# Optimization experiments

Hardware: AMD Instinct MI355X
Metric: run time of the kernel (lower is better)

Reference implementation:

```python
import jax, jax.numpy as jnp
import numpy as np

B, N, F_IN, F_OUT = 64, 1024, 200, 200
NEG_SLOPE = 0.2  # PyG GATConv default


def setup_inputs() -> dict:
    key = jax.random.key(0)
    k1, k2, k3, k4, k5 = jax.random.split(key, 5)
    return {
        "x": jax.random.normal(k1, (B, 1, N, F_IN), dtype=jnp.float32),
        "W": jax.random.normal(k2, (F_IN, F_OUT), dtype=jnp.float32) * 0.05,
        "att_src": jax.random.normal(k3, (F_OUT,), dtype=jnp.float32) * 0.05,
        "att_dst": jax.random.normal(k4, (F_OUT,), dtype=jnp.float32) * 0.05,
        "bias": jax.random.normal(k5, (F_OUT,), dtype=jnp.float32) * 0.05,
    }


def reference(x, W, att_src, att_dst, bias):
    # x: [B, 1, N, F_IN]; module flattens to (B*N) nodes but the edge_index
    # only spans node ids 0..N-1 (complete graph minus self loops). PyG's
    # GATConv re-adds self loops for ALL B*N nodes, so:
    #   nodes 0..N-1 : dense softmax attention over all N nodes (incl. self)
    #   nodes >= N   : only the self loop -> out = h_i + bias
    b, _, n, f = x.shape
    xf = x.reshape(b * n, f)
    h = xf @ W                                # [B*N, F_OUT] linear transform

    h0 = h[:n]                                # first graph's nodes
    a_s = h0 @ att_src                        # [N] per-source score
    a_d = h0 @ att_dst                        # [N] per-target score
    # score[i, j] = leaky_relu(a_dst[i] + a_src[j]), softmax over sources j
    scores = jax.nn.leaky_relu(a_d[:, None] + a_s[None, :], negative_slope=NEG_SLOPE)
    alpha = jax.nn.softmax(scores, axis=1)    # [N, N]
    out0 = alpha @ h0 + bias                  # [N, F_OUT]

    out_rest = h[n:] + bias                   # self-loop only -> alpha == 1
    out = jnp.concatenate([out0, out_rest], axis=0)
    return out.reshape(b, n, -1)[:, None]     # [B, 1, N, F_OUT]
```

## Files before the change

kernel.cpp:

```cpp
#include <hip/hip_runtime.h>

#define BATCH 64
#define NNODE 1024
#define FDIM  200
#define MROWS (BATCH * NNODE)
#define NEG_SLOPE 0.2f

#define NKT 7
#define NNT 13

typedef short s16x8 __attribute__((ext_vector_type(8)));
typedef float f32x4 __attribute__((ext_vector_type(4)));


__device__ __forceinline__ unsigned int f2bf(float f) {
    unsigned int u = __float_as_uint(f);
    return (u + 0x7fffu + ((u >> 16) & 1u)) >> 16;
}
__device__ __forceinline__ unsigned int pack2(float a, float b) {
    return f2bf(a) | (f2bf(b) << 16);
}

__global__ __launch_bounds__(64) void k_prep(const float* __restrict__ W,
                                             const float* __restrict__ att_src,
                                             const float* __restrict__ att_dst,
                                             unsigned short* __restrict__ fragW,
                                             float* __restrict__ wsv,
                                             float* __restrict__ wdv)
{
    const int b    = blockIdx.x;
    const int lane = threadIdx.x;

    if (b < 91) {
        const int kt   = b / NNT;
        const int nt   = b - kt * NNT;
        const int n    = nt * 16 + (lane & 15);
        const int kb   = kt * 32 + (lane >> 4) * 8;
        s16x8 v;
        #pragma unroll
        for (int j = 0; j < 8; ++j) {
            int k = kb + j;
            float f = (k < FDIM && n < FDIM) ? W[k * FDIM + n] : 0.f;
            v[j] = (short)f2bf(f);
        }
        ((s16x8*)(fragW + (size_t)b * 512))[lane] = v;
    } else {
        const int kk = b - 91;
        const float* Wr = W + kk * FDIM;
        float ps = 0.f, pd = 0.f;
        #pragma unroll
        for (int i = 0; i < 4; ++i) {
            int n = lane + i * 64;
            if (n < FDIM) {
                float wv = Wr[n];
                ps = fmaf(wv, att_src[n], ps);
                pd = fmaf(wv, att_dst[n], pd);
            }
        }
        #pragma unroll
        for (int off = 32; off; off >>= 1) {
            ps += __shfl_down(ps, off);
            pd += __shfl_down(pd, off);
        }
        if (lane == 0) { wsv[kk] = ps; wdv[kk] = pd; }
    }
}

__global__ __launch_bounds__(256) void k_av(const float* __restrict__ x,
                                            const float* __restrict__ wsv,
                                            const float* __restrict__ wdv,
                                            float* __restrict__ a_s,
                                            float* __restrict__ a_d)
{
    const int tid  = threadIdx.x;
    const int lane = tid & 63;
    const int row  = blockIdx.x * 4 + (tid >> 6);
    const float* xr = x + (size_t)row * FDIM;
    float ss = 0.f, sd = 0.f;
    for (int k = lane; k < FDIM; k += 64) {
        float xv = xr[k];
        ss = fmaf(xv, wsv[k], ss);
        sd = fmaf(xv, wdv[k], sd);
    }
    #pragma unroll
    for (int off = 32; off; off >>= 1) {
        ss += __shfl_down(ss, off);
        sd += __shfl_down(sd, off);
    }
    if (lane == 0) { a_s[row] = ss; a_d[row] = sd; }
}

__global__ __launch_bounds__(64) void k_gemm(const float* __restrict__ x,
                                             const unsigned short* __restrict__ fragW,
                                             const float* __restrict__ bias,
                                             float* __restrict__ out,
                                             unsigned short* __restrict__ h0frag)
{
    __shared__ float scr[16][17];
    const int lane = threadIdx.x;
    const int ln   = lane & 15;
    const int quad = lane >> 4;
    const int R0   = blockIdx.x * 16;

    f32x4 acc[NNT];
    #pragma unroll
    for (int nt = 0; nt < NNT; ++nt) acc[nt] = (f32x4){0.f, 0.f, 0.f, 0.f};

    const float* xrow = x + (size_t)(R0 + ln) * FDIM;

    float4 ar[NKT][2];
    #pragma unroll
    for (int kt = 0; kt < 4; ++kt) {
        const float4* ap = (const float4*)(xrow + kt * 32 + quad * 8);
        ar[kt][0] = ap[0]; ar[kt][1] = ap[1];
    }

    s16x8 bc[NNT], bn[NNT];
    #pragma unroll
    for (int nt = 0; nt < NNT; ++nt)
        bc[nt] = *(const s16x8*)(fragW + ((size_t)nt * 64 + lane) * 8);

    #pragma unroll
    for (int kt = 0; kt < NKT; ++kt) {
        if (kt < NKT - 1) {
            #pragma unroll
            for (int nt = 0; nt < NNT; ++nt)
                bn[nt] = *(const s16x8*)(fragW +
                    ((size_t)((kt + 1) * NNT + nt) * 64 + lane) * 8);
        }
        if (kt + 4 < NKT) {
            int ka = kt + 4;
            if (ka < 6) {
                const float4* ap = (const float4*)(xrow + ka * 32 + quad * 8);
                ar[ka][0] = ap[0]; ar[ka][1] = ap[1];
            } else {
                if (quad == 0) {
                    const float4* ap = (const float4*)(xrow + ka * 32);
                    ar[ka][0] = ap[0]; ar[ka][1] = ap[1];
                } else {
                    ar[ka][0] = make_float4(0.f, 0.f, 0.f, 0.f);
                    ar[ka][1] = make_float4(0.f, 0.f, 0.f, 0.f);
                }
            }
        }
        float4 f0 = ar[kt][0], f1 = ar[kt][1];
        unsigned int au[4] = {pack2(f0.x, f0.y), pack2(f0.z, f0.w),
                              pack2(f1.x, f1.y), pack2(f1.z, f1.w)};
        s16x8 a = *(s16x8*)au;
        #pragma unroll
        for (int nt = 0; nt < NNT; ++nt)
            acc[nt] = __builtin_amdgcn_mfma_f32_16x16x32_bf16(a, bc[nt], acc[nt], 0, 0, 0);
        if (kt < NKT - 1) {
            #pragma unroll
            for (int nt = 0; nt < NNT; ++nt) bc[nt] = bn[nt];
        }
    }

    if (R0 >= NNODE) {
        #pragma unroll
        for (int nt = 0; nt < NNT; ++nt) {
            int col = nt * 16 + ln;
            if (nt < 12 || ln < 8) {
                float bv = bias[col];
                #pragma unroll
                for (int r = 0; r < 4; ++r)
                    out[(size_t)(R0 + quad * 4 + r) * FDIM + col] = acc[nt][r] + bv;
            }
        }
    } else {
        const int kt2 = R0 >> 5;
        const int lo  = (R0 >> 4) & 1;
        for (int nt = 0; nt < NNT; ++nt) {
            #pragma unroll
            for (int r = 0; r < 4; ++r) scr[quad * 4 + r][ln] = acc[nt][r];
            __syncthreads();
            if (lane < 32) {
                int oct = lane >> 4, nl = lane & 15;
                uint4 dv;
                dv.x = pack2(scr[oct * 8 + 0][nl], scr[oct * 8 + 1][nl]);
                dv.y = pack2(scr[oct * 8 + 2][nl], scr[oct * 8 + 3][nl]);
                dv.z = pack2(scr[oct * 8 + 4][nl], scr[oct * 8 + 5][nl]);
                dv.w = pack2(scr[oct * 8 + 6][nl], scr[oct * 8 + 7][nl]);
                *(uint4*)(h0frag + ((size_t)(kt2 * NNT + nt) * 64 + lo * 32 + lane) * 8) = dv;
            }
            __syncthreads();
        }
    }
}

__global__ __launch_bounds__(256) void k_stats(const float* __restrict__ a_s,
                                               const float* __restrict__ a_d,
                                               float* __restrict__ m_out,
                                               float* __restrict__ l_out)
{
    __shared__ float as_s[1024];
    const int tid = threadIdx.x;
    #pragma unroll
    for (int i = 0; i < 4; ++i) as_s[tid + i * 256] = a_s[tid + i * 256];
    __syncthreads();

    const int lane = tid & 63;
    const int row  = blockIdx.x * 4 + (tid >> 6);

    float mx = -1e30f;
    #pragma unroll
    for (int i = 0; i < 16; ++i) mx = fmaxf(mx, as_s[lane + i * 64]);
    #pragma unroll
    for (int off = 32; off; off >>= 1) mx = fmaxf(mx, __shfl_down(mx, off));
    mx = __shfl(mx, 0);

    const float ad = a_d[row];
    float mi = ad + mx; mi = (mi > 0.f) ? mi : NEG_SLOPE * mi;

    float sum = 0.f;
    #pragma unroll
    for (int i = 0; i < 16; ++i) {
        float s = ad + as_s[lane + i * 64];
        s = (s > 0.f) ? s : NEG_SLOPE * s;
        sum += __expf(s - mi);
    }
    #pragma unroll
    for (int off = 32; off; off >>= 1) sum += __shfl_down(sum, off);
    if (lane == 0) { m_out[row] = mi; l_out[row] = sum; }
}

__global__ __launch_bounds__(256) void k_attn(const unsigned short* __restrict__ h0frag,
                                              const float* __restrict__ a_s,
                                              const float* __restrict__ a_d,
                                              const float* __restrict__ m_v,
                                              const float* __restrict__ l_v,
                                              const float* __restrict__ bias,
                                              float* __restrict__ out)
{
    const int tid  = threadIdx.x;
    const int lane = tid & 63;
    const int w    = __builtin_amdgcn_readfirstlane(tid >> 6);
    const int ln   = lane & 15;
    const int quad = lane >> 4;
    const int it   = blockIdx.x / NNT;
    const int nt   = blockIdx.x - it * NNT;
    const int i0   = it * 64 + w * 16;

    const float ad = a_d[i0 + ln];
    const float mi = m_v[i0 + ln];

    f32x4 accA = (f32x4){0.f, 0.f, 0.f, 0.f};
    f32x4 accB = (f32x4){0.f, 0.f, 0.f, 0.f};

    #pragma unroll
    for (int kt2 = 0; kt2 < 32; ++kt2) {
        const float4* ap = (const float4*)(a_s + kt2 * 32 + quad * 8);
        float4 f0 = ap[0], f1 = ap[1];
        float e[8] = {f0.x, f0.y, f0.z, f0.w, f1.x, f1.y, f1.z, f1.w};
        #pragma unroll
        for (int j = 0; j < 8; ++j) {
            float s = ad + e[j];
            s = (s > 0.f) ? s : NEG_SLOPE * s;
            e[j] = __expf(s - mi);
        }
        unsigned int au[4] = {pack2(e[0], e[1]), pack2(e[2], e[3]),
                              pack2(e[4], e[5]), pack2(e[6], e[7])};
        s16x8 afrag = *(s16x8*)au;
        s16x8 b = *(const s16x8*)(h0frag + ((size_t)(kt2 * NNT + nt) * 64 + lane) * 8);
        if (kt2 & 1) accB = __builtin_amdgcn_mfma_f32_16x16x32_bf16(afrag, b, accB, 0, 0, 0);
        else         accA = __builtin_amdgcn_mfma_f32_16x16x32_bf16(afrag, b, accA, 0, 0, 0);
    }

    const int col = nt * 16 + ln;
    if (nt < 12 || ln < 8) {
        float bv = bias[col];
        #pragma unroll
        for (int r = 0; r < 4; ++r) {
            float rl = 1.0f / l_v[i0 + quad * 4 + r];
            out[(size_t)(i0 + quad * 4 + r) * FDIM + col]
                = (accA[r] + accB[r]) * rl + bv;
        }
    }
}

extern "C" void kernel_launch(void* const* d_in, const int* in_sizes, int n_in,
                              void* d_out, int out_size, void* d_ws, size_t ws_size,
                              hipStream_t stream)
{
    const float* x       = (const float*)d_in[0];
    const float* W       = (const float*)d_in[1];
    const float* att_src = (const float*)d_in[2];
    const float* att_dst = (const float*)d_in[3];
    const float* bias    = (const float*)d_in[4];
    float* out = (float*)d_out;
    char*  wsb = (char*)d_ws;

    unsigned short* h0frag = (unsigned short*)(wsb + 0);
    float* a_s   = (float*)(wsb + 425984);
    float* a_d   = (float*)(wsb + 430080);
    float* m_i   = (float*)(wsb + 434176);
    float* l_i   = (float*)(wsb + 438272);
    unsigned short* fragW = (unsigned short*)(wsb + 442368);
    float* wsv   = (float*)(wsb + 535552);
    float* wdv   = (float*)(wsb + 536352);

    k_prep <<<291,        64, 0, stream>>>(W, att_src, att_dst, fragW, wsv, wdv);
    k_av   <<<NNODE / 4, 256, 0, stream>>>(x, wsv, wdv, a_s, a_d);
    k_stats<<<NNODE / 4, 256, 0, stream>>>(a_s, a_d, m_i, l_i);
    k_gemm <<<MROWS / 16, 64, 0, stream>>>(x, fragW, bias, out, h0frag);
    k_attn <<<16 * NNT,  256, 0, stream>>>(h0frag, a_s, a_d, m_i, l_i, bias, out);
}
```

Measured before the change: 143.2 us.

## Stage W fragments in LDS across 4-wave GEMM blocks and split-K attention

The GEMM now uses 256-thread blocks covering 64 rows. The W fragments for each k-tile are staged into double-buffered LDS with global_load_lds and shared by all four waves, instead of each wave loading them into registers. The attention kernel is split along the source dimension into four chunks, which quadruples the number of blocks. Partial results are accumulated with atomicAdd into an output that k_stats pre-fills with the bias. This adds block-level barriers and atomic traffic, and makes the final sum depend on atomic ordering.

```diff
diff --git a/kernel.cpp b/kernel.cpp
--- a/kernel.cpp
+++ b/kernel.cpp
@@ -8,6 +8,8 @@
 
 #define NKT 7
 #define NNT 13
+#define KTBYTES (NNT * 1024)
+#define KSPLIT 4
 
 typedef short s16x8 __attribute__((ext_vector_type(8)));
 typedef float f32x4 __attribute__((ext_vector_type(4)));
@@ -90,23 +92,43 @@
     if (lane == 0) { a_s[row] = ss; a_d[row] = sd; }
 }
 
-__global__ __launch_bounds__(64) void k_gemm(const float* __restrict__ x,
-                                             const unsigned short* __restrict__ fragW,
-                                             const float* __restrict__ bias,
-                                             float* __restrict__ out,
-                                             unsigned short* __restrict__ h0frag)
-{
-    __shared__ float scr[16][17];
-    const int lane = threadIdx.x;
+__global__ __launch_bounds__(256) void k_gemm(const float* __restrict__ x,
+                                              const unsigned short* __restrict__ fragW,
+                                              const float* __restrict__ bias,
+                                              float* __restrict__ out,
+                                              unsigned short* __restrict__ h0frag)
+{
+    __shared__ __align__(16) unsigned short Bs[2][KTBYTES / 2];
+    const int tid  = threadIdx.x;
+    const int lane = tid & 63;
+    const int w    = __builtin_amdgcn_readfirstlane(tid >> 6);
     const int ln   = lane & 15;
     const int quad = lane >> 4;
-    const int R0   = blockIdx.x * 16;
+    const int R0   = blockIdx.x * 64;
+    const int row0 = R0 + w * 16;
+
+#define STAGE(kt_, buf_)                                                      \
+    {                                                                         \
+        const char* gsrc = (const char*)fragW + (size_t)(kt_) * KTBYTES;      \
+        char* lbase = (char*)&Bs[buf_][0];                                    \
+        _Pragma("unroll")                                                     \
+        for (int i = 0; i < 4; ++i) {                                         \
+            int g = i * 4 + w;                                                \
+            if (g < NNT)                                                      \
+                __builtin_amdgcn_global_load_lds(                             \
+                    (const __attribute__((address_space(1))) void*)           \
+                        (gsrc + g * 1024 + lane * 16),                        \
+                    (__attribute__((address_space(3))) void*)                 \
+                        (lbase + g * 1024),                                   \
+                    16, 0, 0);                                                \
+        }                                                                     \
+    }
 
     f32x4 acc[NNT];
     #pragma unroll
     for (int nt = 0; nt < NNT; ++nt) acc[nt] = (f32x4){0.f, 0.f, 0.f, 0.f};
 
-    const float* xrow = x + (size_t)(R0 + ln) * FDIM;
+    const float* xrow = x + (size_t)(row0 + ln) * FDIM;
 
     float4 ar[NKT][2];
     #pragma unroll
@@ -115,19 +137,14 @@
         ar[kt][0] = ap[0]; ar[kt][1] = ap[1];
     }
 
-    s16x8 bc[NNT], bn[NNT];
-    #pragma unroll
-    for (int nt = 0; nt < NNT; ++nt)
-        bc[nt] = *(const s16x8*)(fragW + ((size_t)nt * 64 + lane) * 8);
+    STAGE(0, 0);
+    __syncthreads();
 
     #pragma unroll
     for (int kt = 0; kt < NKT; ++kt) {
-        if (kt < NKT - 1) {
-            #pragma unroll
-            for (int nt = 0; nt < NNT; ++nt)
-                bn[nt] = *(const s16x8*)(fragW +
-                    ((size_t)((kt + 1) * NNT + nt) * 64 + lane) * 8);
-        }
+        const int cur = kt & 1;
+        if (kt < NKT - 1) STAGE(kt + 1, cur ^ 1);
+
         if (kt + 4 < NKT) {
             int ka = kt + 4;
             if (ka < 6) {
@@ -147,14 +164,16 @@
         unsigned int au[4] = {pack2(f0.x, f0.y), pack2(f0.z, f0.w),
                               pack2(f1.x, f1.y), pack2(f1.z, f1.w)};
         s16x8 a = *(s16x8*)au;
-        #pragma unroll
-        for (int nt = 0; nt < NNT; ++nt)
-            acc[nt] = __builtin_amdgcn_mfma_f32_16x16x32_bf16(a, bc[nt], acc[nt], 0, 0, 0);
-        if (kt < NKT - 1) {
-            #pragma unroll
-            for (int nt = 0; nt < NNT; ++nt) bc[nt] = bn[nt];
-        }
-    }
+
+        const unsigned short* bbase = &Bs[cur][0];
+        #pragma unroll
+        for (int nt = 0; nt < NNT; ++nt) {
+            s16x8 b = *(const s16x8*)(bbase + nt * 512 + lane * 8);
+            acc[nt] = __builtin_amdgcn_mfma_f32_16x16x32_bf16(a, b, acc[nt], 0, 0, 0);
+        }
+        if (kt < NKT - 1) __syncthreads();
+    }
+#undef STAGE
 
     if (R0 >= NNODE) {
         #pragma unroll
@@ -164,23 +183,25 @@
                 float bv = bias[col];
                 #pragma unroll
                 for (int r = 0; r < 4; ++r)
-                    out[(size_t)(R0 + quad * 4 + r) * FDIM + col] = acc[nt][r] + bv;
+                    out[(size_t)(row0 + quad * 4 + r) * FDIM + col] = acc[nt][r] + bv;
             }
         }
     } else {
-        const int kt2 = R0 >> 5;
-        const int lo  = (R0 >> 4) & 1;
+        __syncthreads();
+        float* scrw = (float*)&Bs[0][0] + w * (16 * 17);
+        const int kt2 = row0 >> 5;
+        const int lo  = (row0 >> 4) & 1;
         for (int nt = 0; nt < NNT; ++nt) {
             #pragma unroll
-            for (int r = 0; r < 4; ++r) scr[quad * 4 + r][ln] = acc[nt][r];
+            for (int r = 0; r < 4; ++r) scrw[(quad * 4 + r) * 17 + ln] = acc[nt][r];
             __syncthreads();
             if (lane < 32) {
                 int oct = lane >> 4, nl = lane & 15;
                 uint4 dv;
-                dv.x = pack2(scr[oct * 8 + 0][nl], scr[oct * 8 + 1][nl]);
-                dv.y = pack2(scr[oct * 8 + 2][nl], scr[oct * 8 + 3][nl]);
-                dv.z = pack2(scr[oct * 8 + 4][nl], scr[oct * 8 + 5][nl]);
-                dv.w = pack2(scr[oct * 8 + 6][nl], scr[oct * 8 + 7][nl]);
+                dv.x = pack2(scrw[(oct * 8 + 0) * 17 + nl], scrw[(oct * 8 + 1) * 17 + nl]);
+                dv.y = pack2(scrw[(oct * 8 + 2) * 17 + nl], scrw[(oct * 8 + 3) * 17 + nl]);
+                dv.z = pack2(scrw[(oct * 8 + 4) * 17 + nl], scrw[(oct * 8 + 5) * 17 + nl]);
+                dv.w = pack2(scrw[(oct * 8 + 6) * 17 + nl], scrw[(oct * 8 + 7) * 17 + nl]);
                 *(uint4*)(h0frag + ((size_t)(kt2 * NNT + nt) * 64 + lo * 32 + lane) * 8) = dv;
             }
             __syncthreads();
@@ -190,11 +211,21 @@
 
 __global__ __launch_bounds__(256) void k_stats(const float* __restrict__ a_s,
                                                const float* __restrict__ a_d,
+                                               const float* __restrict__ bias,
+                                               float* __restrict__ out,
                                                float* __restrict__ m_out,
                                                float* __restrict__ l_out)
 {
     __shared__ float as_s[1024];
     const int tid = threadIdx.x;
+
+    if (tid < FDIM) {
+        float bv = bias[tid];
+        #pragma unroll
+        for (int r = 0; r < 4; ++r)
+            out[(size_t)(blockIdx.x * 4 + r) * FDIM + tid] = bv;
+    }
+
     #pragma unroll
     for (int i = 0; i < 4; ++i) as_s[tid + i * 256] = a_s[tid + i * 256];
     __syncthreads();
@@ -229,7 +260,6 @@
                                               const float* __restrict__ a_d,
                                               const float* __restrict__ m_v,
                                               const float* __restrict__ l_v,
-                                              const float* __restrict__ bias,
                                               float* __restrict__ out)
 {
     const int tid  = threadIdx.x;
@@ -237,8 +267,11 @@
     const int w    = __builtin_amdgcn_readfirstlane(tid >> 6);
     const int ln   = lane & 15;
     const int quad = lane >> 4;
-    const int it   = blockIdx.x / NNT;
-    const int nt   = blockIdx.x - it * NNT;
+    const int bid  = blockIdx.x;
+    const int kh   = bid / (16 * NNT);
+    const int r2   = bid - kh * (16 * NNT);
+    const int it   = r2 / NNT;
+    const int nt   = r2 - it * NNT;
     const int i0   = it * 64 + w * 16;
 
     const float ad = a_d[i0 + ln];
@@ -248,7 +281,8 @@
     f32x4 accB = (f32x4){0.f, 0.f, 0.f, 0.f};
 
     #pragma unroll
-    for (int kt2 = 0; kt2 < 32; ++kt2) {
+    for (int k8 = 0; k8 < 8; ++k8) {
+        const int kt2 = kh * 8 + k8;
         const float4* ap = (const float4*)(a_s + kt2 * 32 + quad * 8);
         float4 f0 = ap[0], f1 = ap[1];
         float e[8] = {f0.x, f0.y, f0.z, f0.w, f1.x, f1.y, f1.z, f1.w};
@@ -262,18 +296,17 @@
                               pack2(e[4], e[5]), pack2(e[6], e[7])};
         s16x8 afrag = *(s16x8*)au;
         s16x8 b = *(const s16x8*)(h0frag + ((size_t)(kt2 * NNT + nt) * 64 + lane) * 8);
-        if (kt2 & 1) accB = __builtin_amdgcn_mfma_f32_16x16x32_bf16(afrag, b, accB, 0, 0, 0);
-        else         accA = __builtin_amdgcn_mfma_f32_16x16x32_bf16(afrag, b, accA, 0, 0, 0);
+        if (k8 & 1) accB = __builtin_amdgcn_mfma_f32_16x16x32_bf16(afrag, b, accB, 0, 0, 0);
+        else        accA = __builtin_amdgcn_mfma_f32_16x16x32_bf16(afrag, b, accA, 0, 0, 0);
     }
 
     const int col = nt * 16 + ln;
     if (nt < 12 || ln < 8) {
-        float bv = bias[col];
         #pragma unroll
         for (int r = 0; r < 4; ++r) {
             float rl = 1.0f / l_v[i0 + quad * 4 + r];
-            out[(size_t)(i0 + quad * 4 + r) * FDIM + col]
-                = (accA[r] + accB[r]) * rl + bv;
+            atomicAdd(&out[(size_t)(i0 + quad * 4 + r) * FDIM + col],
+                      (accA[r] + accB[r]) * rl);
         }
     }
 }
@@ -299,9 +332,9 @@
     float* wsv   = (float*)(wsb + 535552);
     float* wdv   = (float*)(wsb + 536352);
 
-    k_prep <<<291,        64, 0, stream>>>(W, att_src, att_dst, fragW, wsv, wdv);
-    k_av   <<<NNODE / 4, 256, 0, stream>>>(x, wsv, wdv, a_s, a_d);
-    k_stats<<<NNODE / 4, 256, 0, stream>>>(a_s, a_d, m_i, l_i);
-    k_gemm <<<MROWS / 16, 64, 0, stream>>>(x, fragW, bias, out, h0frag);
-    k_attn <<<16 * NNT,  256, 0, stream>>>(h0frag, a_s, a_d, m_i, l_i, bias, out);
-}
+    k_prep <<<291,           64, 0, stream>>>(W, att_src, att_dst, fragW, wsv, wdv);
+    k_av   <<<NNODE / 4,    256, 0, stream>>>(x, wsv, wdv, a_s, a_d);
+    k_stats<<<NNODE / 4,    256, 0, stream>>>(a_s, a_d, bias, out, m_i, l_i);
+    k_gemm <<<MROWS / 64,   256, 0, stream>>>(x, fragW, bias, out, h0frag);
+    k_attn <<<KSPLIT * 16 * NNT, 256, 0, stream>>>(h0frag, a_s, a_d, m_i, l_i, out);
+}
```

After: 134.4 us. -6.2%, faster.
